# Kernel optimization log

Measured on AMD Instinct MI355X. Metric: run time of the kernel, lower is better.

The kernel has to match this reference:

```python
import jax, jax.numpy as jnp
import numpy as np

N = 4096            # tokens (dim 0 of x)
LATENT = 1024       # latent_vector_size
H = 16              # num_heads
DK = 64             # key_dim
DV = 64             # val_dim
MHK = H * DK        # 1024, width of q and k blocks


def setup_inputs() -> dict:
    key = jax.random.key(0)
    ks = jax.random.split(key, 5)
    return {
        "x": jax.random.normal(ks[0], (N, LATENT), dtype=jnp.float32),
        "w_qkv": jax.random.normal(ks[1], (LATENT, H * (2 * DK + DV)), dtype=jnp.float32) * (1.0 / np.sqrt(LATENT)),
        "b_qkv": jax.random.normal(ks[2], (H * (2 * DK + DV),), dtype=jnp.float32) * 0.01,
        "w_out": jax.random.normal(ks[3], (H * DV, LATENT), dtype=jnp.float32) * (1.0 / np.sqrt(H * DV)),
        "b_out": jax.random.normal(ks[4], (LATENT,), dtype=jnp.float32) * 0.01,
    }


def reference(x, w_qkv, b_qkv, w_out, b_out):
    # qkv projection: [N, H*(2*Dk+Dv)]
    qkv = x @ w_qkv + b_qkv
    # NOTE: the original module does NOT split into heads; q/k/v are the
    # concatenated head dims and a single [N, N] score matrix is formed,
    # scaled by sqrt(key_dim) (per-head dim), not sqrt(H*key_dim).
    q = qkv[:, :MHK]                 # [N, H*Dk]
    k = qkv[:, MHK:2 * MHK]          # [N, H*Dk]
    v = qkv[:, 2 * MHK:]             # [N, H*Dv]
    scores = (q @ k.T) * (1.0 / jnp.sqrt(jnp.float32(DK)))  # [N, N]
    attn = jax.nn.softmax(scores, axis=-1)
    out = attn @ v                   # [N, H*Dv]
    return out @ w_out + b_out       # [N, LATENT]
```

## Files before the change

### kernel.cpp

```cpp
#include <hip/hip_runtime.h>
#include <hip/hip_fp16.h>


typedef _Float16 half_t;
typedef _Float16 half8 __attribute__((ext_vector_type(8)));
typedef _Float16 half4 __attribute__((ext_vector_type(4)));
typedef float f32x4 __attribute__((ext_vector_type(4)));

static constexpr int N_TOK = 4096;
static constexpr int LATENT = 1024;
static constexpr int QKVN = 3072;

#define DEVI __device__ __forceinline__

DEVI void gld_lds16(const half_t* g, half_t* l) {
  __builtin_amdgcn_global_load_lds(
      (const __attribute__((address_space(1))) void*)g,
      (__attribute__((address_space(3))) void*)l,
      16, 0, 0);
}

DEVI f32x4 MFMA(half8 a, half8 b, f32x4 c) {
  return __builtin_amdgcn_mfma_f32_16x16x32_f16(a, b, c, 0, 0, 0);
}


DEVI void stageH(const half_t* __restrict__ g, int ld, half_t* lbase, int tid) {
#pragma unroll
  for (int i = 0; i < 2; ++i) {
    int c = tid + i * 512;
    int r = c >> 2;
    int k8 = ((c & 3) ^ ((r >> 1) & 3)) * 8;
    gld_lds16(g + (size_t)r * ld + k8, lbase + c * 8);
  }
}

template <int MODE>
__launch_bounds__(512, 2)
__global__ void gemm8(const half_t* __restrict__ A, int lda,
                      const half_t* __restrict__ B, int ldb,
                      void* __restrict__ Cout, int ldc,
                      const float* __restrict__ bias, int K) {
  __shared__ half_t Alds[2][2][256 * 32];
  __shared__ half_t Blds[2][2][256 * 32];

  const int tid = threadIdx.x;
  const int lane = tid & 63;
  const int wid = tid >> 6;

  const int nx = gridDim.x;
  const int nwg = nx * gridDim.y;
  const int bid = blockIdx.y * nx + blockIdx.x;
  const int cpx = nwg >> 3;
  const int swz = (bid & 7) * cpx + (bid >> 3);
  const int rowBlk = (swz / nx) * 256;
  const int colBlk = (swz % nx) * 256;

  const int wr = (wid >> 2) * 128;
  const int wc = (wid & 3) * 64;
  const int fr = lane & 15;
  const int fs = lane >> 4;

  const int kOff = blockIdx.z * K;
  const half_t* Ag = A + (size_t)rowBlk * lda + kOff;
  const half_t* Bg = B + (size_t)colBlk * ldb + kOff;

  f32x4 acc[8][4] = {};
  const int NT = K >> 6;

  stageH(Ag, lda, Alds[0][0], tid);
  stageH(Bg, ldb, Blds[0][0], tid);
  stageH(Ag + 32, lda, Alds[0][1], tid);
  stageH(Bg + 32, ldb, Blds[0][1], tid);
  asm volatile("s_waitcnt vmcnt(4)" ::: "memory");
  __builtin_amdgcn_s_barrier();

  for (int kt = 0; kt < NT; ++kt) {
    const int b = kt & 1;
    const bool st = (kt + 1 < NT);
    const half_t* A0 = Alds[b][0];
    const half_t* B0 = Blds[b][0];
    const half_t* A1 = Alds[b][1];
    const half_t* B1 = Blds[b][1];
    const half_t* AgN = Ag + (kt + 1) * 64;
    const half_t* BgN = Bg + (kt + 1) * 64;

    half8 af[8], bf[4];

#pragma unroll
    for (int m = 0; m < 8; ++m) {
      int row = wr + m * 16 + fr;
      af[m] = *(const half8*)(A0 + row * 32 + ((fs ^ ((row >> 1) & 3)) * 8));
    }
#pragma unroll
    for (int n = 0; n < 2; ++n) {
      int row = wc + n * 16 + fr;
      bf[n] = *(const half8*)(B0 + row * 32 + ((fs ^ ((row >> 1) & 3)) * 8));
    }
    if (st) stageH(AgN, lda, Alds[b ^ 1][0], tid);
    __builtin_amdgcn_s_barrier();
    __builtin_amdgcn_s_setprio(1);
#pragma unroll
    for (int m = 0; m < 8; ++m) {
      acc[m][0] = MFMA(af[m], bf[0], acc[m][0]);
      acc[m][1] = MFMA(af[m], bf[1], acc[m][1]);
    }
    __builtin_amdgcn_s_setprio(0);
    __builtin_amdgcn_s_barrier();

#pragma unroll
    for (int n = 2; n < 4; ++n) {
      int row = wc + n * 16 + fr;
      bf[n] = *(const half8*)(B0 + row * 32 + ((fs ^ ((row >> 1) & 3)) * 8));
    }
    if (st) stageH(BgN, ldb, Blds[b ^ 1][0], tid);
    __builtin_amdgcn_s_barrier();
    __builtin_amdgcn_s_setprio(1);
#pragma unroll
    for (int m = 0; m < 8; ++m) {
      acc[m][2] = MFMA(af[m], bf[2], acc[m][2]);
      acc[m][3] = MFMA(af[m], bf[3], acc[m][3]);
    }
    __builtin_amdgcn_s_setprio(0);
    if (st) asm volatile("s_waitcnt vmcnt(4)" ::: "memory");
    else    asm volatile("s_waitcnt vmcnt(0)" ::: "memory");
    __builtin_amdgcn_s_barrier();

#pragma unroll
    for (int m = 0; m < 8; ++m) {
      int row = wr + m * 16 + fr;
      af[m] = *(const half8*)(A1 + row * 32 + ((fs ^ ((row >> 1) & 3)) * 8));
    }
#pragma unroll
    for (int n = 0; n < 2; ++n) {
      int row = wc + n * 16 + fr;
      bf[n] = *(const half8*)(B1 + row * 32 + ((fs ^ ((row >> 1) & 3)) * 8));
    }
    if (st) stageH(AgN + 32, lda, Alds[b ^ 1][1], tid);
    __builtin_amdgcn_s_barrier();
    __builtin_amdgcn_s_setprio(1);
#pragma unroll
    for (int m = 0; m < 8; ++m) {
      acc[m][0] = MFMA(af[m], bf[0], acc[m][0]);
      acc[m][1] = MFMA(af[m], bf[1], acc[m][1]);
    }
    __builtin_amdgcn_s_setprio(0);
    __builtin_amdgcn_s_barrier();

#pragma unroll
    for (int n = 2; n < 4; ++n) {
      int row = wc + n * 16 + fr;
      bf[n] = *(const half8*)(B1 + row * 32 + ((fs ^ ((row >> 1) & 3)) * 8));
    }
    if (st) stageH(BgN + 32, ldb, Blds[b ^ 1][1], tid);
    __builtin_amdgcn_s_barrier();
    __builtin_amdgcn_s_setprio(1);
#pragma unroll
    for (int m = 0; m < 8; ++m) {
      acc[m][2] = MFMA(af[m], bf[2], acc[m][2]);
      acc[m][3] = MFMA(af[m], bf[3], acc[m][3]);
    }
    __builtin_amdgcn_s_setprio(0);
    if (st) asm volatile("s_waitcnt vmcnt(4)" ::: "memory");
    __builtin_amdgcn_s_barrier();
  }

  const size_t zoff = (MODE == 2) ? (size_t)blockIdx.z * N_TOK * ldc : 0;
#pragma unroll
  for (int m = 0; m < 8; ++m) {
#pragma unroll
    for (int n = 0; n < 4; ++n) {
#pragma unroll
      for (int j = 0; j < 4; ++j) {
        int row = rowBlk + wr + m * 16 + (lane >> 4) * 4 + j;
        int col = colBlk + wc + n * 16 + fr;
        float v = acc[m][n][j];
        if (MODE == 0) {
          v += bias[col];
          if (col < 1024) v *= 0.125f;
          ((half_t*)Cout)[(size_t)row * ldc + col] = (half_t)v;
        } else if (MODE == 1) {
          ((half_t*)Cout)[(size_t)row * ldc + col] = (half_t)v;
        } else {
          ((float*)Cout)[zoff + (size_t)row * ldc + col] = v;
        }
      }
    }
  }
}

template <int ROWS>
DEVI void stage32(const half_t* __restrict__ g, int ld, half_t* lbase, int tid) {
#pragma unroll
  for (int c = tid; c < ROWS * 4; c += 256) {
    int r = c >> 2;
    int k8 = ((c & 3) ^ ((r >> 1) & 3)) * 8;
    gld_lds16(g + (size_t)r * ld + k8, lbase + c * 8);
  }
}

__launch_bounds__(256, 2)
__global__ void gemm2(const half_t* __restrict__ A, int lda,
                      const half_t* __restrict__ B, int ldb,
                      half_t* __restrict__ Cout, int ldc, int K) {
  constexpr int BM = 128, BN = 128, MF = 4, NF = 4;
  __shared__ half_t At[2][BM * 32];
  __shared__ half_t Bt[2][BN * 32];

  const int tid = threadIdx.x;
  const int lane = tid & 63;
  const int wid = tid >> 6;

  const int nx = gridDim.x;
  const int nwg = nx * gridDim.y;
  const int bid = blockIdx.y * nx + blockIdx.x;
  const int cpx = nwg >> 3;
  const int swz = (bid & 7) * cpx + (bid >> 3);
  const int rowBlk = (swz / nx) * BM;
  const int colBlk = (swz % nx) * BN;

  const int wr = (wid >> 1) * (BM / 2);
  const int wc = (wid & 1) * (BN / 2);
  const int fr = lane & 15;
  const int fs = lane >> 4;

  const half_t* Ag = A + (size_t)rowBlk * lda;
  const half_t* Bg = B + (size_t)colBlk * ldb;

  f32x4 acc[MF][NF] = {};
  const int NT = K >> 5;
  stage32<BM>(Ag, lda, At[0], tid);
  stage32<BN>(Bg, ldb, Bt[0], tid);
  __syncthreads();

  int cur = 0;
  for (int t = 0; t < NT; ++t) {
    if (t + 1 < NT) {
      stage32<BM>(Ag + (t + 1) * 32, lda, At[cur ^ 1], tid);
      stage32<BN>(Bg + (t + 1) * 32, ldb, Bt[cur ^ 1], tid);
    }
    const half_t* Ac = At[cur];
    const half_t* Bc = Bt[cur];
    half8 af[MF], bf[NF];
#pragma unroll
    for (int m = 0; m < MF; ++m) {
      int row = wr + m * 16 + fr;
      af[m] = *(const half8*)(Ac + row * 32 + ((fs ^ ((row >> 1) & 3)) * 8));
    }
#pragma unroll
    for (int n = 0; n < NF; ++n) {
      int row = wc + n * 16 + fr;
      bf[n] = *(const half8*)(Bc + row * 32 + ((fs ^ ((row >> 1) & 3)) * 8));
    }
#pragma unroll
    for (int m = 0; m < MF; ++m)
#pragma unroll
      for (int n = 0; n < NF; ++n)
        acc[m][n] = MFMA(af[m], bf[n], acc[m][n]);
    __syncthreads();
    cur ^= 1;
  }

#pragma unroll
  for (int m = 0; m < MF; ++m)
#pragma unroll
    for (int n = 0; n < NF; ++n)
#pragma unroll
      for (int j = 0; j < 4; ++j) {
        int row = rowBlk + wr + m * 16 + (lane >> 4) * 4 + j;
        int col = colBlk + wc + n * 16 + fr;
        Cout[(size_t)row * ldc + col] = (half_t)acc[m][n][j];
      }
}

__launch_bounds__(256)
__global__ void reduce_bias4(const float* __restrict__ p, const float* __restrict__ bias,
                             float* __restrict__ out) {
  int i = blockIdx.x * 256 + threadIdx.x;
  const size_t stride4 = (size_t)N_TOK * LATENT / 4;
  float4 a = ((const float4*)p)[i];
  float4 b = ((const float4*)p)[i + stride4];
  float4 c = ((const float4*)p)[i + 2 * stride4];
  float4 d = ((const float4*)p)[i + 3 * stride4];
  float4 e = ((const float4*)bias)[i & 255];
  float4 r;
  r.x = a.x + b.x + c.x + d.x + e.x;
  r.y = a.y + b.y + c.y + d.y + e.y;
  r.z = a.z + b.z + c.z + d.z + e.z;
  r.w = a.w + b.w + c.w + d.w + e.w;
  ((float4*)out)[i] = r;
}

__launch_bounds__(256)
__global__ void softmax_rows(const half_t* __restrict__ S, half_t* __restrict__ P) {
  const int row = blockIdx.x;
  const int t = threadIdx.x;
  const half8* s8 = (const half8*)(S + (size_t)row * N_TOK);

  half8 v[2];
  float lmax = -1e30f;
#pragma unroll
  for (int i = 0; i < 2; ++i) {
    v[i] = s8[t + i * 256];
#pragma unroll
    for (int j = 0; j < 8; ++j) lmax = fmaxf(lmax, (float)v[i][j]);
  }
#pragma unroll
  for (int off = 32; off; off >>= 1) lmax = fmaxf(lmax, __shfl_xor(lmax, off));

  __shared__ float redm[4];
  __shared__ float reds[4];
  if ((t & 63) == 0) redm[t >> 6] = lmax;
  __syncthreads();
  lmax = fmaxf(fmaxf(redm[0], redm[1]), fmaxf(redm[2], redm[3]));

  float e[16];
  float lsum = 0.f;
#pragma unroll
  for (int i = 0; i < 2; ++i)
#pragma unroll
    for (int j = 0; j < 8; ++j) {
      float ev = __expf((float)v[i][j] - lmax);
      e[i * 8 + j] = ev;
      lsum += ev;
    }
#pragma unroll
  for (int off = 32; off; off >>= 1) lsum += __shfl_xor(lsum, off);
  if ((t & 63) == 0) reds[t >> 6] = lsum;
  __syncthreads();
  float inv = 1.f / (reds[0] + reds[1] + reds[2] + reds[3]);

  half8* p8 = (half8*)(P + (size_t)row * N_TOK);
#pragma unroll
  for (int i = 0; i < 2; ++i) {
    half8 h;
#pragma unroll
    for (int j = 0; j < 8; ++j) h[j] = (half_t)(e[i * 8 + j] * inv);
    p8[t + i * 256] = h;
  }
}

template <typename TI>
__global__ void transpose_to_f16(const TI* __restrict__ in, int ldin,
                                 half_t* __restrict__ out, int ldout) {
  __shared__ float tile[32][33];
  const int cb = blockIdx.x * 32;
  const int rb = blockIdx.y * 32;
  const int tx = threadIdx.x;
#pragma unroll
  for (int i = threadIdx.y; i < 32; i += 8)
    tile[i][tx] = (float)in[(size_t)(rb + i) * ldin + cb + tx];
  __syncthreads();
#pragma unroll
  for (int i = threadIdx.y; i < 32; i += 8)
    out[(size_t)(cb + i) * ldout + rb + tx] = (half_t)tile[tx][i];
}

__global__ void cvt_f32_f16(const float* __restrict__ in, half_t* __restrict__ out) {
  int i = blockIdx.x * 256 + threadIdx.x;
  float4 v = ((const float4*)in)[i];
  half4 h;
  h[0] = (half_t)v.x; h[1] = (half_t)v.y; h[2] = (half_t)v.z; h[3] = (half_t)v.w;
  ((half4*)out)[i] = h;
}

extern "C" void kernel_launch(void* const* d_in, const int* in_sizes, int n_in,
                              void* d_out, int out_size, void* d_ws, size_t ws_size,
                              hipStream_t stream) {
  const float* x = (const float*)d_in[0];
  const float* w_qkv = (const float*)d_in[1];
  const float* b_qkv = (const float*)d_in[2];
  const float* w_out = (const float*)d_in[3];
  const float* b_out = (const float*)d_in[4];
  float* out = (float*)d_out;

  char* ws = (char*)d_ws;
  half_t* xb    = (half_t*)(ws);
  half_t* wqkvT = (half_t*)(ws + ((size_t)8 << 20));
  half_t* qkv   = (half_t*)(ws + ((size_t)14 << 20));
  half_t* S     = (half_t*)(ws + ((size_t)46 << 20));
  half_t* P     = (half_t*)(ws + ((size_t)78 << 20));
  half_t* vwT   = (half_t*)(ws + ((size_t)118 << 20));
  half_t* woutT = (half_t*)(ws + ((size_t)126 << 20));
  float*  parts = (float*)(ws + ((size_t)14 << 20));

  dim3 tb(32, 8);

  cvt_f32_f16<<<(N_TOK * LATENT) / (256 * 4), 256, 0, stream>>>(x, xb);
  transpose_to_f16<float><<<dim3(QKVN / 32, LATENT / 32), tb, 0, stream>>>(w_qkv, QKVN, wqkvT, LATENT);
  transpose_to_f16<float><<<dim3(LATENT / 32, LATENT / 32), tb, 0, stream>>>(w_out, LATENT, woutT, LATENT);
  gemm8<0><<<dim3(QKVN / 256, N_TOK / 256), 512, 0, stream>>>(
      xb, LATENT, wqkvT, LATENT, qkv, QKVN, b_qkv, LATENT);
  gemm2<<<dim3(N_TOK / 128, LATENT / 128), 256, 0, stream>>>(
      woutT, LATENT, qkv + 2 * LATENT, QKVN, vwT, N_TOK, LATENT);
  gemm8<1><<<dim3(N_TOK / 256, N_TOK / 256), 512, 0, stream>>>(
      qkv, QKVN, qkv + LATENT, QKVN, S, N_TOK, nullptr, LATENT);
  softmax_rows<<<N_TOK, 256, 0, stream>>>(S, P);
  gemm8<2><<<dim3(LATENT / 256, N_TOK / 256, 4), 512, 0, stream>>>(
      P, N_TOK, vwT, N_TOK, parts, LATENT, nullptr, 1024);
  reduce_bias4<<<(N_TOK * LATENT) / (256 * 4), 256, 0, stream>>>(parts, b_out, out);
}
```

Before: 184.7 us.

## Store split-K partials in fp16 and merge gemm8 k-loop into per-half phases

Changes the split-K partial outputs of the final GEMM from fp32 to fp16, halving the write and read traffic of the partial buffer, and adapts the reduce kernel to read half8 and process 8 elements per thread. It also restructures the gemm8 main loop: instead of four sub-phases with separate A/B staging and barriers, each k-half loads all B fragments, stages both A and B for the next tile, then issues all 32 MFMAs. This cuts barriers but raises register pressure, reduces interleaving of loads with compute, and loses precision in the partial sums.

```diff
diff --git a/kernel.cpp b/kernel.cpp
--- a/kernel.cpp
+++ b/kernel.cpp
@@ -78,91 +78,41 @@
   for (int kt = 0; kt < NT; ++kt) {
     const int b = kt & 1;
     const bool st = (kt + 1 < NT);
-    const half_t* A0 = Alds[b][0];
-    const half_t* B0 = Blds[b][0];
-    const half_t* A1 = Alds[b][1];
-    const half_t* B1 = Blds[b][1];
     const half_t* AgN = Ag + (kt + 1) * 64;
     const half_t* BgN = Bg + (kt + 1) * 64;
 
     half8 af[8], bf[4];
 
 #pragma unroll
-    for (int m = 0; m < 8; ++m) {
-      int row = wr + m * 16 + fr;
-      af[m] = *(const half8*)(A0 + row * 32 + ((fs ^ ((row >> 1) & 3)) * 8));
-    }
-#pragma unroll
-    for (int n = 0; n < 2; ++n) {
-      int row = wc + n * 16 + fr;
-      bf[n] = *(const half8*)(B0 + row * 32 + ((fs ^ ((row >> 1) & 3)) * 8));
-    }
-    if (st) stageH(AgN, lda, Alds[b ^ 1][0], tid);
-    __builtin_amdgcn_s_barrier();
-    __builtin_amdgcn_s_setprio(1);
-#pragma unroll
-    for (int m = 0; m < 8; ++m) {
-      acc[m][0] = MFMA(af[m], bf[0], acc[m][0]);
-      acc[m][1] = MFMA(af[m], bf[1], acc[m][1]);
-    }
-    __builtin_amdgcn_s_setprio(0);
-    __builtin_amdgcn_s_barrier();
-
-#pragma unroll
-    for (int n = 2; n < 4; ++n) {
-      int row = wc + n * 16 + fr;
-      bf[n] = *(const half8*)(B0 + row * 32 + ((fs ^ ((row >> 1) & 3)) * 8));
-    }
-    if (st) stageH(BgN, ldb, Blds[b ^ 1][0], tid);
-    __builtin_amdgcn_s_barrier();
-    __builtin_amdgcn_s_setprio(1);
-#pragma unroll
-    for (int m = 0; m < 8; ++m) {
-      acc[m][2] = MFMA(af[m], bf[2], acc[m][2]);
-      acc[m][3] = MFMA(af[m], bf[3], acc[m][3]);
-    }
-    __builtin_amdgcn_s_setprio(0);
-    if (st) asm volatile("s_waitcnt vmcnt(4)" ::: "memory");
-    else    asm volatile("s_waitcnt vmcnt(0)" ::: "memory");
-    __builtin_amdgcn_s_barrier();
-
-#pragma unroll
-    for (int m = 0; m < 8; ++m) {
-      int row = wr + m * 16 + fr;
-      af[m] = *(const half8*)(A1 + row * 32 + ((fs ^ ((row >> 1) & 3)) * 8));
-    }
-#pragma unroll
-    for (int n = 0; n < 2; ++n) {
-      int row = wc + n * 16 + fr;
-      bf[n] = *(const half8*)(B1 + row * 32 + ((fs ^ ((row >> 1) & 3)) * 8));
-    }
-    if (st) stageH(AgN + 32, lda, Alds[b ^ 1][1], tid);
-    __builtin_amdgcn_s_barrier();
-    __builtin_amdgcn_s_setprio(1);
-#pragma unroll
-    for (int m = 0; m < 8; ++m) {
-      acc[m][0] = MFMA(af[m], bf[0], acc[m][0]);
-      acc[m][1] = MFMA(af[m], bf[1], acc[m][1]);
-    }
-    __builtin_amdgcn_s_setprio(0);
-    __builtin_amdgcn_s_barrier();
-
-#pragma unroll
-    for (int n = 2; n < 4; ++n) {
-      int row = wc + n * 16 + fr;
-      bf[n] = *(const half8*)(B1 + row * 32 + ((fs ^ ((row >> 1) & 3)) * 8));
-    }
-    if (st) stageH(BgN + 32, ldb, Blds[b ^ 1][1], tid);
-    __builtin_amdgcn_s_barrier();
-    __builtin_amdgcn_s_setprio(1);
-#pragma unroll
-    for (int m = 0; m < 8; ++m) {
-      acc[m][2] = MFMA(af[m], bf[2], acc[m][2]);
-      acc[m][3] = MFMA(af[m], bf[3], acc[m][3]);
-    }
-    __builtin_amdgcn_s_setprio(0);
-    if (st) asm volatile("s_waitcnt vmcnt(4)" ::: "memory");
-    __builtin_amdgcn_s_barrier();
+    for (int kh = 0; kh < 2; ++kh) {
+      const half_t* Ac = Alds[b][kh];
+      const half_t* Bc = Blds[b][kh];
+#pragma unroll
+      for (int m = 0; m < 8; ++m) {
+        int row = wr + m * 16 + fr;
+        af[m] = *(const half8*)(Ac + row * 32 + ((fs ^ ((row >> 1) & 3)) * 8));
+      }
+#pragma unroll
+      for (int n = 0; n < 4; ++n) {
+        int row = wc + n * 16 + fr;
+        bf[n] = *(const half8*)(Bc + row * 32 + ((fs ^ ((row >> 1) & 3)) * 8));
+      }
+      if (st) {
+        stageH(AgN + kh * 32, lda, Alds[b ^ 1][kh], tid);
+        stageH(BgN + kh * 32, ldb, Blds[b ^ 1][kh], tid);
+      }
+      __builtin_amdgcn_s_barrier();
+      __builtin_amdgcn_s_setprio(1);
+#pragma unroll
+      for (int m = 0; m < 8; ++m)
+#pragma unroll
+        for (int n = 0; n < 4; ++n)
+          acc[m][n] = MFMA(af[m], bf[n], acc[m][n]);
+      __builtin_amdgcn_s_setprio(0);
+      if (st) asm volatile("s_waitcnt vmcnt(4)" ::: "memory");
+      else if (kh == 0) asm volatile("s_waitcnt vmcnt(0)" ::: "memory");
+      __builtin_amdgcn_s_barrier();
+    }
   }
 
   const size_t zoff = (MODE == 2) ? (size_t)blockIdx.z * N_TOK * ldc : 0;
@@ -182,7 +132,7 @@
         } else if (MODE == 1) {
           ((half_t*)Cout)[(size_t)row * ldc + col] = (half_t)v;
         } else {
-          ((float*)Cout)[zoff + (size_t)row * ldc + col] = v;
+          ((half_t*)Cout)[zoff + (size_t)row * ldc + col] = (half_t)v;
         }
       }
     }
@@ -274,21 +224,25 @@
 }
 
 __launch_bounds__(256)
-__global__ void reduce_bias4(const float* __restrict__ p, const float* __restrict__ bias,
+__global__ void reduce_bias4(const half_t* __restrict__ p, const float* __restrict__ bias,
                              float* __restrict__ out) {
   int i = blockIdx.x * 256 + threadIdx.x;
-  const size_t stride4 = (size_t)N_TOK * LATENT / 4;
-  float4 a = ((const float4*)p)[i];
-  float4 b = ((const float4*)p)[i + stride4];
-  float4 c = ((const float4*)p)[i + 2 * stride4];
-  float4 d = ((const float4*)p)[i + 3 * stride4];
-  float4 e = ((const float4*)bias)[i & 255];
-  float4 r;
-  r.x = a.x + b.x + c.x + d.x + e.x;
-  r.y = a.y + b.y + c.y + d.y + e.y;
-  r.z = a.z + b.z + c.z + d.z + e.z;
-  r.w = a.w + b.w + c.w + d.w + e.w;
-  ((float4*)out)[i] = r;
+  const size_t stride8 = (size_t)N_TOK * LATENT / 8;
+  half8 a = ((const half8*)p)[i];
+  half8 b = ((const half8*)p)[i + stride8];
+  half8 c = ((const half8*)p)[i + 2 * stride8];
+  half8 d = ((const half8*)p)[i + 3 * stride8];
+  float4 e0 = ((const float4*)bias)[(i & 127) * 2];
+  float4 e1 = ((const float4*)bias)[(i & 127) * 2 + 1];
+  float r[8];
+#pragma unroll
+  for (int j = 0; j < 8; ++j)
+    r[j] = (float)a[j] + (float)b[j] + (float)c[j] + (float)d[j];
+  float4 o0, o1;
+  o0.x = r[0] + e0.x; o0.y = r[1] + e0.y; o0.z = r[2] + e0.z; o0.w = r[3] + e0.w;
+  o1.x = r[4] + e1.x; o1.y = r[5] + e1.y; o1.z = r[6] + e1.z; o1.w = r[7] + e1.w;
+  ((float4*)out)[i * 2] = o0;
+  ((float4*)out)[i * 2 + 1] = o1;
 }
 
 __launch_bounds__(256)
@@ -382,7 +336,7 @@
   half_t* P     = (half_t*)(ws + ((size_t)78 << 20));
   half_t* vwT   = (half_t*)(ws + ((size_t)118 << 20));
   half_t* woutT = (half_t*)(ws + ((size_t)126 << 20));
-  float*  parts = (float*)(ws + ((size_t)14 << 20));
+  half_t* parts = (half_t*)(ws + ((size_t)14 << 20));
 
   dim3 tb(32, 8);
 
@@ -398,5 +352,5 @@
   softmax_rows<<<N_TOK, 256, 0, stream>>>(S, P);
   gemm8<2><<<dim3(LATENT / 256, N_TOK / 256, 4), 512, 0, stream>>>(
       P, N_TOK, vwT, N_TOK, parts, LATENT, nullptr, 1024);
-  reduce_bias4<<<(N_TOK * LATENT) / (256 * 4), 256, 0, stream>>>(parts, b_out, out);
-}
+  reduce_bias4<<<(N_TOK * LATENT) / (256 * 8), 256, 0, stream>>>(parts, b_out, out);
+}
```

Result: faster. 172.6 us (-6.5%).
